# Kernel optimization log

Measured on AMD Instinct MI355X. Metric: run time of the kernel, lower is better.

The kernel has to match this reference:

```python
import jax, jax.numpy as jnp
import numpy as np

N_ATOMS = 100_000
N_EDGES = 6_400_000
N_MOL = 128
Z_MAX = 90
KE = 14.3996
CUTOFF = 5.0


def setup_inputs() -> dict:
    key = jax.random.key(0)
    ks = jax.random.split(key, 9)
    partial_charges = jax.random.normal(ks[0], (N_ATOMS,), dtype=jnp.float32)
    Z = jax.random.randint(ks[1], (N_ATOMS,), 0, Z_MAX, dtype=jnp.int32)
    # Born exponents typically ~6-12
    ns = jax.random.uniform(ks[2], (N_ATOMS,), dtype=jnp.float32) * 4.0 + 6.0
    idx_m = jnp.sort(jax.random.randint(ks[3], (N_ATOMS,), 0, N_MOL, dtype=jnp.int32))
    idx_m = idx_m.at[-1].set(N_MOL - 1)
    # displacement vectors with norms bounded away from 0 to keep 1/d^n finite in fp32
    dirs = jax.random.normal(ks[4], (N_EDGES, 3), dtype=jnp.float32)
    dirs = dirs / jnp.linalg.norm(dirs, axis=1, keepdims=True)
    lengths = jax.random.uniform(ks[5], (N_EDGES, 1), dtype=jnp.float32) * 4.5 + 1.0
    Rij = dirs * lengths
    idx_i = jax.random.randint(ks[6], (N_EDGES,), 0, N_ATOMS, dtype=jnp.int32)
    idx_j = jax.random.randint(ks[7], (N_EDGES,), 0, N_ATOMS, dtype=jnp.int32)
    is_film = jax.random.randint(ks[8], (N_ATOMS,), 0, 2, dtype=jnp.int32)
    # dense realization of r0_dict: keyed by (is_film_i, is_film_j, Z_i, Z_j)
    r0_table = jax.random.uniform(jax.random.fold_in(key, 99), (2, 2, Z_MAX, Z_MAX), dtype=jnp.float32) * 1.5 + 0.5
    return {
        "partial_charges": partial_charges, "Z": Z, "ns": ns, "idx_m": idx_m,
        "Rij": Rij, "idx_i": idx_i, "idx_j": idx_j, "is_film": is_film,
        "r0_table": r0_table,
    }


def reference(partial_charges, Z, ns, idx_m, Rij, idx_i, idx_j, is_film, r0_table):
    q = partial_charges
    q_ij = jnp.abs(q[idx_i] * q[idx_j])                      # [E]
    d_ij = jnp.linalg.norm(Rij, axis=1)                      # [E]
    n_ij = ns[idx_i] + ns[idx_j] / 2.0                       # [E]
    r0_ij = r0_table[is_film[idx_i], is_film[idx_j], Z[idx_i], Z[idx_j]]  # [E]
    B_ij = q_ij * r0_ij ** (n_ij - 1.0) / n_ij               # [E]
    # shifted Born potential: B * (1/d^n - 1/cutoff^n)
    potential = B_ij * (d_ij ** (-n_ij) - CUTOFF ** (-n_ij))
    potential = jnp.where(d_ij <= CUTOFF, potential, jnp.zeros_like(potential))
    y = jax.ops.segment_sum(potential, idx_i, num_segments=N_ATOMS)  # edge -> atom
    y = jax.ops.segment_sum(y, idx_m, num_segments=N_MOL)            # atom -> molecule
    return 0.5 * KE * y
```

## Files before the change

kernel.cpp:

```cpp
#include <hip/hip_runtime.h>

#define NMOL 128
#define ZMAX 90
#define BLOCK_E 256
#define GRID_E 2048
#define BLOCK_P 256

typedef float  fx4 __attribute__((ext_vector_type(4)));
typedef int    ix4 __attribute__((ext_vector_type(4)));

__device__ __forceinline__ float fast_exp2(float x) {
#if __has_builtin(__builtin_amdgcn_exp2f)
    return __builtin_amdgcn_exp2f(x);
#else
    return exp2f(x);
#endif
}
__device__ __forceinline__ float fast_log2(float x) {
#if __has_builtin(__builtin_amdgcn_logf)
    return __builtin_amdgcn_logf(x);
#else
    return log2f(x);
#endif
}
__device__ __forceinline__ float fast_rcp(float x) {
#if __has_builtin(__builtin_amdgcn_rcpf)
    return __builtin_amdgcn_rcpf(x);
#else
    return 1.0f / x;
#endif
}

__global__ void pack_atoms_kernel(const float* __restrict__ q,
                                  const int* __restrict__ Z,
                                  const float* __restrict__ ns,
                                  const int* __restrict__ idx_m,
                                  const int* __restrict__ is_film,
                                  float4* __restrict__ atoms,
                                  float* __restrict__ out, int nA) {
    int t = blockIdx.x * BLOCK_P + threadIdx.x;
    if (blockIdx.x == 0 && threadIdx.x < NMOL) out[threadIdx.x] = 0.0f;
    if (t < nA) {
        float4 a;
        a.x = q[t];
        a.y = ns[t];
        a.z = __int_as_float(Z[t] | (is_film[t] << 16));
        a.w = __int_as_float(idx_m[t]);
        atoms[t] = a;
    }
}

__device__ __forceinline__ float pot_from(const float4& ai, const float4& aj,
                                          float r0, float d2) {
    constexpr float LOG2_CUT = 2.321928094887362f;
    const float qij = fabsf(ai.x * aj.x);
    const float n = fmaf(0.5f, aj.y, ai.y);
    const float B = qij * fast_exp2((n - 1.0f) * fast_log2(r0)) * fast_rcp(n);
    const float dpow = fast_exp2(-0.5f * n * fast_log2(d2));
    const float cpow = fast_exp2(-n * LOG2_CUT);
    return (d2 <= 25.0f) ? B * (dpow - cpow) : 0.0f;
}

__device__ __forceinline__ int tbl_idx(const float4& ai, const float4& aj) {
    int zi = __float_as_int(ai.z);
    int zj = __float_as_int(aj.z);
    const int fi = zi >> 16, fj = zj >> 16;
    zi &= 0xFFFF; zj &= 0xFFFF;
    return ((fi * 2 + fj) * ZMAX + zi) * ZMAX + zj;
}

__global__ void __launch_bounds__(BLOCK_E, 8)
edge_kernel(const float4* __restrict__ atoms,
            const float* __restrict__ r0_table,
            const fx4* __restrict__ Rij4,
            const ix4* __restrict__ idx_i4,
            const ix4* __restrict__ idx_j4,
            float* __restrict__ out, int nE) {
    constexpr float HALF_KE = 7.1998f;

    __shared__ float bins[NMOL];
    for (int t = threadIdx.x; t < NMOL; t += BLOCK_E) bins[t] = 0.0f;
    __syncthreads();

    const int nE4 = nE >> 2;
    const int stride = gridDim.x * BLOCK_E;
    for (int t = blockIdx.x * BLOCK_E + threadIdx.x; t < nE4; t += stride) {
        const ix4 ii = __builtin_nontemporal_load(&idx_i4[t]);
        const ix4 jj = __builtin_nontemporal_load(&idx_j4[t]);
        const fx4 ra = __builtin_nontemporal_load(&Rij4[3 * t + 0]);
        const fx4 rb = __builtin_nontemporal_load(&Rij4[3 * t + 1]);
        const fx4 rc = __builtin_nontemporal_load(&Rij4[3 * t + 2]);

        const float4 a0 = atoms[ii.x];
        const float4 a1 = atoms[ii.y];
        const float4 a2 = atoms[ii.z];
        const float4 a3 = atoms[ii.w];
        const float4 b0 = atoms[jj.x];
        const float4 b1 = atoms[jj.y];
        const float4 b2 = atoms[jj.z];
        const float4 b3 = atoms[jj.w];

        const float d20 = fmaf(ra.x, ra.x, fmaf(ra.y, ra.y, ra.z * ra.z));
        const float d21 = fmaf(ra.w, ra.w, fmaf(rb.x, rb.x, rb.y * rb.y));
        const float d22 = fmaf(rb.z, rb.z, fmaf(rb.w, rb.w, rc.x * rc.x));
        const float d23 = fmaf(rc.y, rc.y, fmaf(rc.z, rc.z, rc.w * rc.w));

        const float r00 = r0_table[tbl_idx(a0, b0)];
        const float r01 = r0_table[tbl_idx(a1, b1)];
        const float r02 = r0_table[tbl_idx(a2, b2)];
        const float r03 = r0_table[tbl_idx(a3, b3)];

        const float p0 = pot_from(a0, b0, r00, d20);
        const float p1 = pot_from(a1, b1, r01, d21);
        const float p2 = pot_from(a2, b2, r02, d22);
        const float p3 = pot_from(a3, b3, r03, d23);

        if (p0 != 0.0f) atomicAdd(&bins[__float_as_int(a0.w)], p0);
        if (p1 != 0.0f) atomicAdd(&bins[__float_as_int(a1.w)], p1);
        if (p2 != 0.0f) atomicAdd(&bins[__float_as_int(a2.w)], p2);
        if (p3 != 0.0f) atomicAdd(&bins[__float_as_int(a3.w)], p3);
    }

    const int tail_start = nE4 << 2;
    const int* idx_i = (const int*)idx_i4;
    const int* idx_j = (const int*)idx_j4;
    const float* Rij = (const float*)Rij4;
    for (int e = tail_start + blockIdx.x * BLOCK_E + threadIdx.x; e < nE; e += stride) {
        const float4 ai = atoms[idx_i[e]];
        const float4 aj = atoms[idx_j[e]];
        const float x = Rij[3 * e + 0], y = Rij[3 * e + 1], z = Rij[3 * e + 2];
        const float d2 = fmaf(x, x, fmaf(y, y, z * z));
        const float p = pot_from(ai, aj, r0_table[tbl_idx(ai, aj)], d2);
        if (p != 0.0f) atomicAdd(&bins[__float_as_int(ai.w)], p);
    }

    __syncthreads();
    for (int t = threadIdx.x; t < NMOL; t += BLOCK_E) {
        const float v = bins[t];
        if (v != 0.0f) atomicAdd(&out[t], v * HALF_KE);
    }
}

__global__ void __launch_bounds__(BLOCK_P)
edge_kernel_raw(const float* __restrict__ q,
                const int* __restrict__ Z,
                const float* __restrict__ ns,
                const int* __restrict__ idx_m,
                const int* __restrict__ is_film,
                const float* __restrict__ r0_table,
                const float* __restrict__ Rij,
                const int* __restrict__ idx_i,
                const int* __restrict__ idx_j,
                float* __restrict__ out, int nE) {
    constexpr float HALF_KE = 7.1998f;
    constexpr float LOG2_CUT = 2.321928094887362f;

    __shared__ float bins[NMOL];
    for (int t = threadIdx.x; t < NMOL; t += BLOCK_P) bins[t] = 0.0f;
    __syncthreads();

    const int stride = gridDim.x * BLOCK_P;
    for (int e = blockIdx.x * BLOCK_P + threadIdx.x; e < nE; e += stride) {
        const int i = idx_i[e];
        const int j = idx_j[e];
        const float x = Rij[3 * e + 0], y = Rij[3 * e + 1], z = Rij[3 * e + 2];
        const float d2 = fmaf(x, x, fmaf(y, y, z * z));
        const float r0 = r0_table[((is_film[i] * 2 + is_film[j]) * ZMAX + Z[i]) * ZMAX + Z[j]];
        const float qij = fabsf(q[i] * q[j]);
        const float n = fmaf(0.5f, ns[j], ns[i]);
        const float B = qij * fast_exp2((n - 1.0f) * fast_log2(r0)) * fast_rcp(n);
        const float dpow = fast_exp2(-0.5f * n * fast_log2(d2));
        const float cpow = fast_exp2(-n * LOG2_CUT);
        if (d2 <= 25.0f) atomicAdd(&bins[idx_m[i]], B * (dpow - cpow));
    }

    __syncthreads();
    for (int t = threadIdx.x; t < NMOL; t += BLOCK_P) {
        const float v = bins[t];
        if (v != 0.0f) atomicAdd(&out[t], v * HALF_KE);
    }
}

__global__ void zero_out_kernel(float* __restrict__ out) {
    if (threadIdx.x < NMOL) out[threadIdx.x] = 0.0f;
}

extern "C" void kernel_launch(void* const* d_in, const int* in_sizes, int n_in,
                              void* d_out, int out_size, void* d_ws, size_t ws_size,
                              hipStream_t stream) {
    const float* q        = (const float*)d_in[0];
    const int*   Z        = (const int*)  d_in[1];
    const float* ns       = (const float*)d_in[2];
    const int*   idx_m    = (const int*)  d_in[3];
    const float* Rij      = (const float*)d_in[4];
    const int*   idx_i    = (const int*)  d_in[5];
    const int*   idx_j    = (const int*)  d_in[6];
    const int*   is_film  = (const int*)  d_in[7];
    const float* r0_table = (const float*)d_in[8];

    const int nA = in_sizes[0];
    const int nE = in_sizes[5];
    float* out = (float*)d_out;

    const size_t atoms_bytes = (size_t)nA * sizeof(float4);

    if (ws_size >= atoms_bytes) {
        float4* atoms = (float4*)d_ws;
        const int pack_grid = (nA + BLOCK_P - 1) / BLOCK_P;
        pack_atoms_kernel<<<pack_grid, BLOCK_P, 0, stream>>>(q, Z, ns, idx_m, is_film,
                                                             atoms, out, nA);
        edge_kernel<<<GRID_E, BLOCK_E, 0, stream>>>(atoms, r0_table,
                                                    (const fx4*)Rij,
                                                    (const ix4*)idx_i,
                                                    (const ix4*)idx_j,
                                                    out, nE);
    } else {
        zero_out_kernel<<<1, BLOCK_P, 0, stream>>>(out);
        edge_kernel_raw<<<2048, BLOCK_P, 0, stream>>>(q, Z, ns, idx_m, is_film, r0_table,
                                                      Rij, idx_i, idx_j, out, nE);
    }
}
```

Measured before the change: 246.1 us.

## Stage log2 of r0 table as quantized shorts in LDS and fold exponentials

```diff
diff --git a/kernel.cpp b/kernel.cpp
--- a/kernel.cpp
+++ b/kernel.cpp
@@ -2,8 +2,9 @@
 
 #define NMOL 128
 #define ZMAX 90
-#define BLOCK_E 256
-#define GRID_E 2048
+#define TBL (2 * 2 * ZMAX * ZMAX)
+#define BLOCK_E 1024
+#define GRID_E 512
 #define BLOCK_P 256
 
 typedef float  fx4 __attribute__((ext_vector_type(4)));
@@ -50,15 +51,15 @@
     }
 }
 
-__device__ __forceinline__ float pot_from(const float4& ai, const float4& aj,
-                                          float r0, float d2) {
-    constexpr float LOG2_CUT = 2.321928094887362f;
-    const float qij = fabsf(ai.x * aj.x);
-    const float n = fmaf(0.5f, aj.y, ai.y);
-    const float B = qij * fast_exp2((n - 1.0f) * fast_log2(r0)) * fast_rcp(n);
-    const float dpow = fast_exp2(-0.5f * n * fast_log2(d2));
-    const float cpow = fast_exp2(-n * LOG2_CUT);
-    return (d2 <= 25.0f) ? B * (dpow - cpow) : 0.0f;
+__global__ void build_tbl_kernel(const float* __restrict__ r0_table,
+                                 short* __restrict__ tbl_q, int n) {
+    int t = blockIdx.x * blockDim.x + threadIdx.x;
+    if (t < n) {
+        float v = log2f(r0_table[t]) * 32768.0f;
+        int iv = (int)lrintf(v);
+        iv = min(32767, max(-32768, iv));
+        tbl_q[t] = (short)iv;
+    }
 }
 
 __device__ __forceinline__ int tbl_idx(const float4& ai, const float4& aj) {
@@ -69,16 +70,36 @@
     return ((fi * 2 + fj) * ZMAX + zi) * ZMAX + zj;
 }
 
+__device__ __forceinline__ float pot_from(const float4& ai, const float4& aj,
+                                          float t, float d2) {
+    constexpr float LOG2_CUT = 2.321928094887362f;
+    const float qij = fabsf(ai.x * aj.x);
+    const float n = fmaf(0.5f, aj.y, ai.y);
+    const float bexp = (n - 1.0f) * t;
+    const float e1 = fmaf(-0.5f * n, fast_log2(d2), bexp);
+    const float e2 = fmaf(-n, LOG2_CUT, bexp);
+    const float p = qij * fast_rcp(n) * (fast_exp2(e1) - fast_exp2(e2));
+    return (d2 <= 25.0f) ? p : 0.0f;
+}
+
 __global__ void __launch_bounds__(BLOCK_E, 8)
 edge_kernel(const float4* __restrict__ atoms,
-            const float* __restrict__ r0_table,
+            const short* __restrict__ tbl_q,
             const fx4* __restrict__ Rij4,
             const ix4* __restrict__ idx_i4,
             const ix4* __restrict__ idx_j4,
             float* __restrict__ out, int nE) {
     constexpr float HALF_KE = 7.1998f;
-
+    constexpr float ISCALE = 3.0517578125e-05f;
+
+    __shared__ short r0l[TBL];
     __shared__ float bins[NMOL];
+
+    {
+        const ix4* src = (const ix4*)tbl_q;
+        ix4* dst = (ix4*)r0l;
+        for (int t = threadIdx.x; t < TBL * 2 / 16; t += BLOCK_E) dst[t] = src[t];
+    }
     for (int t = threadIdx.x; t < NMOL; t += BLOCK_E) bins[t] = 0.0f;
     __syncthreads();
 
@@ -105,15 +126,15 @@
         const float d22 = fmaf(rb.z, rb.z, fmaf(rb.w, rb.w, rc.x * rc.x));
         const float d23 = fmaf(rc.y, rc.y, fmaf(rc.z, rc.z, rc.w * rc.w));
 
-        const float r00 = r0_table[tbl_idx(a0, b0)];
-        const float r01 = r0_table[tbl_idx(a1, b1)];
-        const float r02 = r0_table[tbl_idx(a2, b2)];
-        const float r03 = r0_table[tbl_idx(a3, b3)];
-
-        const float p0 = pot_from(a0, b0, r00, d20);
-        const float p1 = pot_from(a1, b1, r01, d21);
-        const float p2 = pot_from(a2, b2, r02, d22);
-        const float p3 = pot_from(a3, b3, r03, d23);
+        const float t0 = (float)r0l[tbl_idx(a0, b0)] * ISCALE;
+        const float t1 = (float)r0l[tbl_idx(a1, b1)] * ISCALE;
+        const float t2 = (float)r0l[tbl_idx(a2, b2)] * ISCALE;
+        const float t3 = (float)r0l[tbl_idx(a3, b3)] * ISCALE;
+
+        const float p0 = pot_from(a0, b0, t0, d20);
+        const float p1 = pot_from(a1, b1, t1, d21);
+        const float p2 = pot_from(a2, b2, t2, d22);
+        const float p3 = pot_from(a3, b3, t3, d23);
 
         if (p0 != 0.0f) atomicAdd(&bins[__float_as_int(a0.w)], p0);
         if (p1 != 0.0f) atomicAdd(&bins[__float_as_int(a1.w)], p1);
@@ -130,7 +151,8 @@
         const float4 aj = atoms[idx_j[e]];
         const float x = Rij[3 * e + 0], y = Rij[3 * e + 1], z = Rij[3 * e + 2];
         const float d2 = fmaf(x, x, fmaf(y, y, z * z));
-        const float p = pot_from(ai, aj, r0_table[tbl_idx(ai, aj)], d2);
+        const float tt = (float)r0l[tbl_idx(ai, aj)] * ISCALE;
+        const float p = pot_from(ai, aj, tt, d2);
         if (p != 0.0f) atomicAdd(&bins[__float_as_int(ai.w)], p);
     }
 
@@ -203,13 +225,16 @@
     float* out = (float*)d_out;
 
     const size_t atoms_bytes = (size_t)nA * sizeof(float4);
-
-    if (ws_size >= atoms_bytes) {
+    const size_t tbl_bytes = (size_t)TBL * sizeof(short);
+
+    if (ws_size >= atoms_bytes + tbl_bytes) {
         float4* atoms = (float4*)d_ws;
+        short* tbl_q = (short*)((char*)d_ws + atoms_bytes);
         const int pack_grid = (nA + BLOCK_P - 1) / BLOCK_P;
         pack_atoms_kernel<<<pack_grid, BLOCK_P, 0, stream>>>(q, Z, ns, idx_m, is_film,
                                                              atoms, out, nA);
-        edge_kernel<<<GRID_E, BLOCK_E, 0, stream>>>(atoms, r0_table,
+        build_tbl_kernel<<<(TBL + 255) / 256, 256, 0, stream>>>(r0_table, tbl_q, TBL);
+        edge_kernel<<<GRID_E, BLOCK_E, 0, stream>>>(atoms, tbl_q,
                                                     (const fx4*)Rij,
                                                     (const ix4*)idx_i,
                                                     (const ix4*)idx_j,
```

Result: faster. 236.3 us (-4.0%).
